# Kernel tuning notes

Measured on AMD Instinct MI355X. Metric: run time of the kernel, lower is better.

Reference implementation:

```python
import jax, jax.numpy as jnp
import numpy as np

N, E, F, H, EA = 50000, 640000, 128, 128, 8


def setup_inputs() -> dict:
    key = jax.random.key(0)
    ks = jax.random.split(key, 16)
    s = 0.05
    return {
        "h": jax.random.normal(ks[0], (N, F), jnp.float32),
        "pos": jax.random.normal(ks[1], (N, 3), jnp.float32),
        "edge_index": jax.random.randint(ks[2], (2, E), 0, N, jnp.int32),
        "edge_attr": jax.random.normal(ks[3], (E, EA), jnp.float32),
        # edge_mlp_1: in = 2F + 1 + EA
        "eW1": jax.random.normal(ks[4], (2 * F + 1 + EA, H), jnp.float32) * s,
        "eb1": jnp.zeros((H,), jnp.float32),
        "eW2": jax.random.normal(ks[5], (H, H), jnp.float32) * s,
        "eb2": jnp.zeros((H,), jnp.float32),
        "aW": jax.random.normal(ks[6], (H, 1), jnp.float32) * s,
        "ab": jnp.zeros((1,), jnp.float32),
        "nW1": jax.random.normal(ks[7], (H + F, H), jnp.float32) * s,
        "nb1": jnp.zeros((H,), jnp.float32),
        "nW2": jax.random.normal(ks[8], (H, F), jnp.float32) * s,
        "nb2": jnp.zeros((F,), jnp.float32),
        # pos_mlp_2: xavier with gain 0.001 -> tiny init, no bias
        "pW2": jax.random.normal(ks[9], (H, 1), jnp.float32) * 0.001,
    }


def reference(h, pos, edge_index, edge_attr,
              eW1, eb1, eW2, eb2, aW, ab,
              nW1, nb1, nW2, nb2, pW2):
    n = h.shape[0]
    row, col = edge_index[0], edge_index[1]
    # radial info
    pos_diff = pos[row] - pos[col]                      # [E,3]
    dist_sq = jnp.sum(pos_diff * pos_diff, axis=-1, keepdims=True)  # [E,1]
    # edge model (Eq.3): gather -> MLP -> sigmoid attention gate
    e_in = jnp.concatenate([h[row], h[col], dist_sq, edge_attr], axis=-1)
    m = jax.nn.silu(e_in @ eW1 + eb1)
    m = jax.nn.silu(m @ eW2 + eb2)
    m = m * jax.nn.sigmoid(m @ aW + ab)                 # [E,H]
    # pos model (note: original overwrites pos_mlp_1 output; faithful to that)
    trans = pos_diff * (m @ pW2)                        # [E,3]
    agg_t = jax.ops.segment_sum(trans, row, num_segments=n)
    cnt = jax.ops.segment_sum(jnp.ones((trans.shape[0], 1), trans.dtype), row,
                              num_segments=n)
    pos_new = pos + agg_t / jnp.maximum(cnt, 1.0)       # unsorted_segment_mean
    # node model: scatter-sum aggregate -> MLP -> residual
    agg = jax.ops.segment_sum(m, row, num_segments=n)   # [N,H]
    o = jax.nn.silu(jnp.concatenate([h, agg], axis=1) @ nW1 + nb1)
    h_new = o @ nW2 + nb2 + h
    return h_new, pos_new, m
```

## Files before the change

### kernel.cpp

```cpp
#include <hip/hip_runtime.h>
#include <hip/hip_bf16.h>

#define NN 50000
#define EE 640000
#define FF 128
#define HH 128

typedef unsigned short ushort_t;
typedef unsigned int   uint_t;
using f32x4  = __attribute__((ext_vector_type(4))) float;
using bf16x8 = __attribute__((ext_vector_type(8))) __bf16;
using u16x8  = __attribute__((ext_vector_type(8))) unsigned short;

__device__ __forceinline__ ushort_t f2bf(float f) {
    union { float f; unsigned int i; } v; v.f = f;
    unsigned int r = v.i + 0x7fffu + ((v.i >> 16) & 1u);
    return (ushort_t)(r >> 16);
}
__device__ __forceinline__ float bf2f(uint_t u) {
    union { uint_t i; float f; } v; v.i = u << 16; return v.f;
}
__device__ __forceinline__ float fsilu(float x) { return x / (1.f + __expf(-x)); }
__device__ __forceinline__ float fsig(float x)  { return 1.f / (1.f + __expf(-x)); }

__device__ __forceinline__ u16x8 cvt8(const float* p) {
    float4 a0 = *reinterpret_cast<const float4*>(p);
    float4 a1 = *reinterpret_cast<const float4*>(p + 4);
    u16x8 v;
    v[0] = f2bf(a0.x); v[1] = f2bf(a0.y); v[2] = f2bf(a0.z); v[3] = f2bf(a0.w);
    v[4] = f2bf(a1.x); v[5] = f2bf(a1.y); v[6] = f2bf(a1.z); v[7] = f2bf(a1.w);
    return v;
}

__device__ __forceinline__ void gld_lds16(const void* g, void* l) {
    typedef const __attribute__((address_space(1))) unsigned int glb_u32;
    typedef __attribute__((address_space(3))) unsigned int lds_u32;
    __builtin_amdgcn_global_load_lds((glb_u32*)g, (lds_u32*)l, 16, 0, 0);
}

__global__ void prep_kernel(const float* __restrict__ h, ushort_t* __restrict__ hbf,
                            const int* __restrict__ eidx, int* __restrict__ deg)
{
    const int t = blockIdx.x * 256 + threadIdx.x;
    if (t * 8 < NN * 128) {
        u16x8 v = cvt8(h + (size_t)t * 8);
        *reinterpret_cast<u16x8*>(hbf + (size_t)t * 8) = v;
    }
    if (t < EE) atomicAdd(&deg[eidx[t]], 1);
}

__global__ void scan_kernel(const int* __restrict__ deg, int* __restrict__ row_ptr,
                            int* __restrict__ cursor)
{
    __shared__ int sdata[1024];
    const int t = threadIdx.x;
    const int chunk = (NN + 1023) / 1024;
    const int start = t * chunk;
    const int end   = min(start + chunk, NN);
    int s = 0;
    for (int i = start; i < end; ++i) s += deg[i];
    sdata[t] = s;
    __syncthreads();
    for (int off = 1; off < 1024; off <<= 1) {
        int v = (t >= off) ? sdata[t - off] : 0;
        __syncthreads();
        sdata[t] += v;
        __syncthreads();
    }
    int ox = sdata[t] - s;
    for (int i = start; i < end; ++i) {
        row_ptr[i] = ox; cursor[i] = ox; ox += deg[i];
    }
    if (t == 1023) row_ptr[NN] = sdata[1023];
}

__global__ void scatter_kernel(const int* __restrict__ eidx, int* __restrict__ cursor,
                               int* __restrict__ edge_list, int* __restrict__ row_sorted)
{
    const int e = blockIdx.x * 256 + threadIdx.x;
    if (e < EE) {
        const int r = eidx[e];
        const int p = atomicAdd(&cursor[r], 1);
        edge_list[p] = e;
        row_sorted[p] = r;
    }
}

#define M_STR 136

__device__ __forceinline__ ushort_t* ah_ptr(ushort_t* base, int row, int b) {
    return base + row * 256 + ((b ^ ((row & 7) << 4)) >> 1);
}

__global__ __launch_bounds__(256, 2) void egcl_edge_kernel(
    const ushort_t* __restrict__ hbf, const float* __restrict__ pos,
    const int* __restrict__ eidx, const float* __restrict__ eattr,
    const int* __restrict__ edge_list, const int* __restrict__ row_sorted,
    const float* __restrict__ w1, const float* __restrict__ b1,
    const float* __restrict__ w2, const float* __restrict__ b2,
    const float* __restrict__ aW, const float* __restrict__ ab,
    const float* __restrict__ pW2,
    float* __restrict__ m_out, float* __restrict__ agg, float* __restrict__ agg_t)
{
    __shared__ __align__(16) ushort_t A_h[64 * 256];
    __shared__ __align__(16) ushort_t A_misc[64 * 16];
    __shared__ __align__(16) ushort_t M1_sh[64 * M_STR];
    __shared__ int   ROW_sh[64];
    __shared__ float GATE_sh[64];

    ushort_t* M2_sh = A_h;

    const int tid  = threadIdx.x;
    const int lane = tid & 63;
    const int w    = tid >> 6;
    const int l15  = lane & 15;
    const int lg   = lane >> 4;

    bf16x8 B1[9][2];
    bf16x8 B2[4][2];
    bf16x8 Bg[4];
    float b1c[2], b2c[2];
    const float abv = ab[0];
#pragma unroll
    for (int nt = 0; nt < 2; ++nt) {
        const int colg = 32 * w + 16 * nt + l15;
        b1c[nt] = b1[colg];
        b2c[nt] = b2[colg];
#pragma unroll
        for (int ks = 0; ks < 9; ++ks) {
            u16x8 v;
#pragma unroll
            for (int j = 0; j < 8; ++j) {
                const int k = 32 * ks + 8 * lg + j;
                v[j] = (k < 265) ? f2bf(w1[k * 128 + colg]) : (ushort_t)0;
            }
            B1[ks][nt] = __builtin_bit_cast(bf16x8, v);
        }
#pragma unroll
        for (int ks = 0; ks < 4; ++ks) {
            u16x8 v;
#pragma unroll
            for (int j = 0; j < 8; ++j) {
                const int k = 32 * ks + 8 * lg + j;
                v[j] = f2bf(w2[k * 128 + colg]);
            }
            B2[ks][nt] = __builtin_bit_cast(bf16x8, v);
        }
    }
#pragma unroll
    for (int ks = 0; ks < 4; ++ks) {
        u16x8 v;
#pragma unroll
        for (int j = 0; j < 8; ++j) {
            const int k = 32 * ks + 8 * lg + j;
            v[j] = (l15 == 0) ? f2bf(aW[k]) : (l15 == 1 ? f2bf(pW2[k]) : (ushort_t)0);
        }
        Bg[ks] = __builtin_bit_cast(bf16x8, v);
    }

    const int ei = tid >> 2;
    const int et = tid & 3;

    for (int tile = blockIdx.x; tile < EE / 64; tile += gridDim.x) {
        const int p  = tile * 64 + ei;
        const int eo = edge_list[p];
        const int r  = row_sorted[p];
        const int c  = eidx[EE + eo];

#pragma unroll
        for (int i = 0; i < 8; ++i) {
            const int rl = 2 * i + (lane >> 5);
            const int bs = (lane & 31) << 4;
            const int b  = bs ^ ((rl & 7) << 4);
            const int rr = __shfl(r, 4 * rl);
            const int cc = __shfl(c, 4 * rl);
            const int node = (b < 256) ? rr : cc;
            const char* src = (const char*)hbf + (size_t)node * 256 + (b & 255);
            gld_lds16(src, (char*)A_h + (w * 8192 + i * 1024));
        }

        float pdx = 0.f, pdy = 0.f, pdz = 0.f;
        if (et == 0) {
            ROW_sh[ei] = r;
            pdx = pos[r * 3 + 0] - pos[c * 3 + 0];
            pdy = pos[r * 3 + 1] - pos[c * 3 + 1];
            pdz = pos[r * 3 + 2] - pos[c * 3 + 2];
            const float ds = pdx * pdx + pdy * pdy + pdz * pdz;
            const float4 ea0 = *reinterpret_cast<const float4*>(eattr + (size_t)eo * 8);
            const float4 ea1 = *reinterpret_cast<const float4*>(eattr + (size_t)eo * 8 + 4);
            u16x8 v0;
            v0[0] = f2bf(ds);
            v0[1] = f2bf(ea0.x); v0[2] = f2bf(ea0.y); v0[3] = f2bf(ea0.z);
            v0[4] = f2bf(ea0.w); v0[5] = f2bf(ea1.x); v0[6] = f2bf(ea1.y);
            v0[7] = f2bf(ea1.z);
            *reinterpret_cast<u16x8*>(&A_misc[ei * 16]) = v0;
            u16x8 v1 = {0, 0, 0, 0, 0, 0, 0, 0};
            v1[0] = f2bf(ea1.w);
            *reinterpret_cast<u16x8*>(&A_misc[ei * 16 + 8]) = v1;
        }
        __syncthreads();

#pragma unroll
        for (int s = 0; s < 4; ++s) {
            f32x4 a0 = {0.f, 0.f, 0.f, 0.f};
            f32x4 a1 = {0.f, 0.f, 0.f, 0.f};
#pragma unroll
            for (int ks = 0; ks < 9; ++ks) {
                bf16x8 a;
                if (ks < 8) {
                    a = *reinterpret_cast<const bf16x8*>(
                        ah_ptr(A_h, 16 * s + l15, 64 * ks + 16 * lg));
                } else if (lg < 2) {
                    a = *reinterpret_cast<const bf16x8*>(
                        &A_misc[(16 * s + l15) * 16 + 8 * lg]);
                } else {
                    u16x8 z = {0, 0, 0, 0, 0, 0, 0, 0};
                    a = __builtin_bit_cast(bf16x8, z);
                }
                a0 = __builtin_amdgcn_mfma_f32_16x16x32_bf16(a, B1[ks][0], a0, 0, 0, 0);
                a1 = __builtin_amdgcn_mfma_f32_16x16x32_bf16(a, B1[ks][1], a1, 0, 0, 0);
            }
#pragma unroll
            for (int nt = 0; nt < 2; ++nt) {
#pragma unroll
                for (int rr2 = 0; rr2 < 4; ++rr2) {
                    const float x = (nt == 0 ? a0[rr2] : a1[rr2]) + b1c[nt];
                    const int edge = 16 * s + 4 * lg + rr2;
                    const int colg = 32 * w + 16 * nt + l15;
                    M1_sh[edge * M_STR + colg] = f2bf(fsilu(x));
                }
            }
        }
        __syncthreads();

#pragma unroll
        for (int s = 0; s < 4; ++s) {
            f32x4 a0 = {0.f, 0.f, 0.f, 0.f};
            f32x4 a1 = {0.f, 0.f, 0.f, 0.f};
#pragma unroll
            for (int ks = 0; ks < 4; ++ks) {
                bf16x8 a = *reinterpret_cast<const bf16x8*>(
                    &M1_sh[(16 * s + l15) * M_STR + ks * 32 + lg * 8]);
                a0 = __builtin_amdgcn_mfma_f32_16x16x32_bf16(a, B2[ks][0], a0, 0, 0, 0);
                a1 = __builtin_amdgcn_mfma_f32_16x16x32_bf16(a, B2[ks][1], a1, 0, 0, 0);
            }
#pragma unroll
            for (int nt = 0; nt < 2; ++nt) {
#pragma unroll
                for (int rr2 = 0; rr2 < 4; ++rr2) {
                    const float x = (nt == 0 ? a0[rr2] : a1[rr2]) + b2c[nt];
                    const int edge = 16 * s + 4 * lg + rr2;
                    const int colg = 32 * w + 16 * nt + l15;
                    M2_sh[edge * M_STR + colg] = f2bf(fsilu(x));
                }
            }
        }
        __syncthreads();

        {
            f32x4 ga = {0.f, 0.f, 0.f, 0.f};
#pragma unroll
            for (int ks = 0; ks < 4; ++ks) {
                bf16x8 a = *reinterpret_cast<const bf16x8*>(
                    &M2_sh[(16 * w + l15) * M_STR + ks * 32 + lg * 8]);
                ga = __builtin_amdgcn_mfma_f32_16x16x32_bf16(a, Bg[ks], ga, 0, 0, 0);
            }
            float gqw[4], txw[4], tyw[4], tzw[4];
#pragma unroll
            for (int rr2 = 0; rr2 < 4; ++rr2) {
                const float sa = __shfl(ga[rr2], lane & 48);
                const float sp = __shfl(ga[rr2], (lane & 48) + 1);
                gqw[rr2] = fsig(sa + abv);
                const float t = gqw[rr2] * sp;
                const float px = __shfl(pdx, 16 * lg + 4 * rr2);
                const float py = __shfl(pdy, 16 * lg + 4 * rr2);
                const float pz = __shfl(pdz, 16 * lg + 4 * rr2);
                txw[rr2] = px * t; tyw[rr2] = py * t; tzw[rr2] = pz * t;
                if (l15 == 0) GATE_sh[16 * w + 4 * lg + rr2] = gqw[rr2];
            }
            if (l15 == 0) {
                int cur = -1; float t0 = 0.f, t1 = 0.f, t2 = 0.f;
#pragma unroll
                for (int rr2 = 0; rr2 < 4; ++rr2) {
                    const int rid = ROW_sh[16 * w + 4 * lg + rr2];
                    if (rid != cur) {
                        if (cur >= 0) {
                            atomicAdd(&agg_t[cur * 3 + 0], t0);
                            atomicAdd(&agg_t[cur * 3 + 1], t1);
                            atomicAdd(&agg_t[cur * 3 + 2], t2);
                        }
                        cur = rid; t0 = t1 = t2 = 0.f;
                    }
                    t0 += txw[rr2]; t1 += tyw[rr2]; t2 += tzw[rr2];
                }
                atomicAdd(&agg_t[cur * 3 + 0], t0);
                atomicAdd(&agg_t[cur * 3 + 1], t1);
                atomicAdd(&agg_t[cur * 3 + 2], t2);
            }
        }
        __syncthreads();

#pragma unroll
        for (int j = 0; j < 16; ++j) {
            const int row = 16 * w + j;
            const int eo2 = edge_list[tile * 64 + row];
            const uint_t pv = *reinterpret_cast<const uint_t*>(&M2_sh[row * M_STR + 2 * lane]);
            const float g = GATE_sh[row];
            float2 st;
            st.x = bf2f(pv & 0xffffu) * g;
            st.y = bf2f(pv >> 16) * g;
            *reinterpret_cast<float2*>(&m_out[(size_t)eo2 * 128 + 2 * lane]) = st;
        }

        {
            const int col = tid & 127;
            const int j0  = (tid >> 7) * 32;
            int cur = ROW_sh[j0];
            float acc = 0.f;
#pragma unroll 4
            for (int j = j0; j < j0 + 32; ++j) {
                const int rid = ROW_sh[j];
                const float v = bf2f((uint_t)M2_sh[j * M_STR + col]) * GATE_sh[j];
                if (rid != cur) {
                    atomicAdd(&agg[(size_t)cur * 128 + col], acc);
                    acc = 0.f; cur = rid;
                }
                acc += v;
            }
            atomicAdd(&agg[(size_t)cur * 128 + col], acc);
        }
        __syncthreads();
    }
}

__global__ __launch_bounds__(256, 4) void egcl_node_kernel(
    const ushort_t* __restrict__ hbf,
    const float* __restrict__ agg, const float* __restrict__ agg_t,
    const int* __restrict__ row_ptr, const float* __restrict__ pos,
    const float* __restrict__ w1, const float* __restrict__ b1,
    const float* __restrict__ w2, const float* __restrict__ b2,
    float* __restrict__ hn_out, float* __restrict__ pos_out)
{
    __shared__ __align__(16) ushort_t A_sh[16 * 264];
    __shared__ __align__(16) ushort_t M1_sh[16 * 136];

    const int tid  = threadIdx.x;
    const int lane = tid & 63;
    const int w    = tid >> 6;
    const int l15  = lane & 15;
    const int lg   = lane >> 4;

    bf16x8 B1[8][2];
    bf16x8 B2[4][2];
    float b1c[2], b2c[2];
#pragma unroll
    for (int nt = 0; nt < 2; ++nt) {
        const int colg = 32 * w + 16 * nt + l15;
        b1c[nt] = b1[colg];
        b2c[nt] = b2[colg];
#pragma unroll
        for (int ks = 0; ks < 8; ++ks) {
            u16x8 v;
#pragma unroll
            for (int j = 0; j < 8; ++j) {
                const int k = 32 * ks + 8 * lg + j;
                v[j] = f2bf(w1[k * 128 + colg]);
            }
            B1[ks][nt] = __builtin_bit_cast(bf16x8, v);
        }
#pragma unroll
        for (int ks = 0; ks < 4; ++ks) {
            u16x8 v;
#pragma unroll
            for (int j = 0; j < 8; ++j) {
                const int k = 32 * ks + 8 * lg + j;
                v[j] = f2bf(w2[k * 128 + colg]);
            }
            B2[ks][nt] = __builtin_bit_cast(bf16x8, v);
        }
    }

    const int ni = tid >> 4;
    const int nt16 = tid & 15;

    for (int tile = blockIdx.x; tile < NN / 16; tile += gridDim.x) {
        __syncthreads();
        const int base = tile * 16;
        {
            const size_t n = (size_t)base + ni;
            *reinterpret_cast<u16x8*>(&A_sh[ni * 264 + nt16 * 8]) =
                *reinterpret_cast<const u16x8*>(hbf + n * 128 + nt16 * 8);
            u16x8 av = cvt8(agg + n * 128 + nt16 * 8);
            *reinterpret_cast<u16x8*>(&A_sh[ni * 264 + 128 + nt16 * 8]) = av;
        }
        if (tid < 48) {
            const int nl = tid / 3, d = tid % 3;
            const size_t n = (size_t)base + nl;
            const float c = (float)(row_ptr[n + 1] - row_ptr[n]);
            pos_out[n * 3 + d] = pos[n * 3 + d] + agg_t[n * 3 + d] / fmaxf(c, 1.f);
        }
        __syncthreads();

        f32x4 acc10 = {0.f, 0.f, 0.f, 0.f};
        f32x4 acc11 = {0.f, 0.f, 0.f, 0.f};
#pragma unroll
        for (int ks = 0; ks < 8; ++ks) {
            bf16x8 a = *reinterpret_cast<const bf16x8*>(&A_sh[l15 * 264 + ks * 32 + lg * 8]);
            acc10 = __builtin_amdgcn_mfma_f32_16x16x32_bf16(a, B1[ks][0], acc10, 0, 0, 0);
            acc11 = __builtin_amdgcn_mfma_f32_16x16x32_bf16(a, B1[ks][1], acc11, 0, 0, 0);
        }
#pragma unroll
        for (int nt = 0; nt < 2; ++nt) {
#pragma unroll
            for (int r = 0; r < 4; ++r) {
                const float x = (nt == 0 ? acc10[r] : acc11[r]) + b1c[nt];
                const int nl = 4 * lg + r;
                const int colg = 32 * w + 16 * nt + l15;
                M1_sh[nl * 136 + colg] = f2bf(fsilu(x));
            }
        }
        __syncthreads();

        f32x4 acc20 = {0.f, 0.f, 0.f, 0.f};
        f32x4 acc21 = {0.f, 0.f, 0.f, 0.f};
#pragma unroll
        for (int ks = 0; ks < 4; ++ks) {
            bf16x8 a = *reinterpret_cast<const bf16x8*>(&M1_sh[l15 * 136 + ks * 32 + lg * 8]);
            acc20 = __builtin_amdgcn_mfma_f32_16x16x32_bf16(a, B2[ks][0], acc20, 0, 0, 0);
            acc21 = __builtin_amdgcn_mfma_f32_16x16x32_bf16(a, B2[ks][1], acc21, 0, 0, 0);
        }
#pragma unroll
        for (int nt = 0; nt < 2; ++nt) {
#pragma unroll
            for (int r = 0; r < 4; ++r) {
                const int nl = 4 * lg + r;
                const int colg = 32 * w + 16 * nt + l15;
                const size_t n = (size_t)base + nl;
                const float hres = bf2f((uint_t)A_sh[nl * 264 + colg]);
                const float y = (nt == 0 ? acc20[r] : acc21[r]) + b2c[nt] + hres;
                hn_out[n * 128 + colg] = y;
            }
        }
    }
}

extern "C" void kernel_launch(void* const* d_in, const int* in_sizes, int n_in,
                              void* d_out, int out_size, void* d_ws, size_t ws_size,
                              hipStream_t stream)
{
    const float* h     = (const float*)d_in[0];
    const float* pos   = (const float*)d_in[1];
    const int*   eidx  = (const int*)d_in[2];
    const float* eattr = (const float*)d_in[3];
    const float* eW1   = (const float*)d_in[4];
    const float* eb1   = (const float*)d_in[5];
    const float* eW2   = (const float*)d_in[6];
    const float* eb2   = (const float*)d_in[7];
    const float* aW    = (const float*)d_in[8];
    const float* ab    = (const float*)d_in[9];
    const float* nW1   = (const float*)d_in[10];
    const float* nb1   = (const float*)d_in[11];
    const float* nW2   = (const float*)d_in[12];
    const float* nb2   = (const float*)d_in[13];
    const float* pW2   = (const float*)d_in[14];

    float* out    = (float*)d_out;
    float* hn_out = out;
    float* po_out = out + (size_t)NN * 128;
    float* m_out  = po_out + (size_t)NN * 3;

    char* wsb = (char*)d_ws;
    float* agg        = (float*)(wsb + 0);
    float* agg_t      = (float*)(wsb + 25600000);
    int*   deg        = (int*)  (wsb + 26200000);
    int*   row_ptr    = (int*)  (wsb + 26400000);
    int*   cursor     = (int*)  (wsb + 26600256);
    int*   edge_list  = (int*)  (wsb + 26800256);
    int*   row_sorted = (int*)  (wsb + 29360256);
    ushort_t* hbf     = (ushort_t*)(wsb + 31920256);

    hipMemsetAsync(wsb, 0, 26400000, stream);

    prep_kernel<<<3200, 256, 0, stream>>>(h, hbf, eidx, deg);
    scan_kernel<<<1, 1024, 0, stream>>>(deg, row_ptr, cursor);
    scatter_kernel<<<(EE + 255) / 256, 256, 0, stream>>>(eidx, cursor, edge_list, row_sorted);

    egcl_edge_kernel<<<512, 256, 0, stream>>>(hbf, pos, eidx, eattr,
                                              edge_list, row_sorted,
                                              eW1, eb1, eW2, eb2, aW, ab, pW2,
                                              m_out, agg, agg_t);
    egcl_node_kernel<<<512, 256, 0, stream>>>(hbf, agg, agg_t, row_ptr, pos,
                                              nW1, nb1, nW2, nb2,
                                              hn_out, po_out);
}
```

Baseline: 519.0 us.

## Prefetch next edge tile, parallelize scan, fold agg zeroing into prep

The single-block serial prefix scan becomes a three-kernel parallel scan. Zeroing agg moves from a large memset into prep_kernel, so the memset only clears agg_t and deg. The edge kernel now issues the next tile's gather loads (do_stage) at the end of each iteration, overlapping them with compute. It also drops a barrier by fusing the m_out store with per-wave segmented atomic aggregation, and lays out M2_sh in per-wave blocks. The changes remove serial scan latency and memset traffic and hide gather latency. The cost is more launches and extra live registers for the prefetched pos_diff values.

```diff
diff --git a/kernel.cpp b/kernel.cpp
--- a/kernel.cpp
+++ b/kernel.cpp
@@ -39,39 +39,65 @@
 }
 
 __global__ void prep_kernel(const float* __restrict__ h, ushort_t* __restrict__ hbf,
-                            const int* __restrict__ eidx, int* __restrict__ deg)
+                            const int* __restrict__ eidx, int* __restrict__ deg,
+                            float* __restrict__ agg)
 {
     const int t = blockIdx.x * 256 + threadIdx.x;
-    if (t * 8 < NN * 128) {
+    if (t < 800000) {
         u16x8 v = cvt8(h + (size_t)t * 8);
         *reinterpret_cast<u16x8*>(hbf + (size_t)t * 8) = v;
+        const float4 z4 = {0.f, 0.f, 0.f, 0.f};
+        *reinterpret_cast<float4*>(agg + (size_t)t * 8)     = z4;
+        *reinterpret_cast<float4*>(agg + (size_t)t * 8 + 4) = z4;
     }
     if (t < EE) atomicAdd(&deg[eidx[t]], 1);
 }
 
-__global__ void scan_kernel(const int* __restrict__ deg, int* __restrict__ row_ptr,
-                            int* __restrict__ cursor)
-{
-    __shared__ int sdata[1024];
+__global__ void scan_local_kernel(const int* __restrict__ deg,
+                                  int* __restrict__ row_ptr, int* __restrict__ bsum)
+{
+    __shared__ int sd[256];
     const int t = threadIdx.x;
-    const int chunk = (NN + 1023) / 1024;
-    const int start = t * chunk;
-    const int end   = min(start + chunk, NN);
-    int s = 0;
-    for (int i = start; i < end; ++i) s += deg[i];
-    sdata[t] = s;
+    const int i = blockIdx.x * 256 + t;
+    const int v = (i < NN) ? deg[i] : 0;
+    sd[t] = v;
     __syncthreads();
-    for (int off = 1; off < 1024; off <<= 1) {
-        int v = (t >= off) ? sdata[t - off] : 0;
-        __syncthreads();
-        sdata[t] += v;
-        __syncthreads();
-    }
-    int ox = sdata[t] - s;
-    for (int i = start; i < end; ++i) {
-        row_ptr[i] = ox; cursor[i] = ox; ox += deg[i];
-    }
-    if (t == 1023) row_ptr[NN] = sdata[1023];
+    for (int off = 1; off < 256; off <<= 1) {
+        const int u = (t >= off) ? sd[t - off] : 0;
+        __syncthreads();
+        sd[t] += u;
+        __syncthreads();
+    }
+    if (i < NN) row_ptr[i] = sd[t] - v;
+    if (t == 255) bsum[blockIdx.x] = sd[255];
+}
+
+__global__ void scan_bsum_kernel(int* __restrict__ bsum)
+{
+    __shared__ int sd[256];
+    const int t = threadIdx.x;
+    const int v = (t < 196) ? bsum[t] : 0;
+    sd[t] = v;
+    __syncthreads();
+    for (int off = 1; off < 256; off <<= 1) {
+        const int u = (t >= off) ? sd[t - off] : 0;
+        __syncthreads();
+        sd[t] += u;
+        __syncthreads();
+    }
+    if (t < 196) bsum[t] = sd[t] - v;
+}
+
+__global__ void scan_fix_kernel(int* __restrict__ row_ptr, const int* __restrict__ bsum,
+                                int* __restrict__ cursor)
+{
+    const int i = blockIdx.x * 256 + threadIdx.x;
+    if (i < NN) {
+        const int p = row_ptr[i] + bsum[blockIdx.x];
+        row_ptr[i] = p;
+        cursor[i]  = p;
+    }
+    if (i == 0) row_ptr[NN] = EE;
 }
 
 __global__ void scatter_kernel(const int* __restrict__ eidx, int* __restrict__ cursor,
@@ -90,6 +116,9 @@
 
 __device__ __forceinline__ ushort_t* ah_ptr(ushort_t* base, int row, int b) {
     return base + row * 256 + ((b ^ ((row & 7) << 4)) >> 1);
+}
+__device__ __forceinline__ int m2_off(int row) {
+    return (row >> 4) * 4096 + (row & 15) * M_STR;
 }
 
 __global__ __launch_bounds__(256, 2) void egcl_edge_kernel(
@@ -160,13 +189,15 @@
 
     const int ei = tid >> 2;
     const int et = tid & 3;
-
-    for (int tile = blockIdx.x; tile < EE / 64; tile += gridDim.x) {
-        const int p  = tile * 64 + ei;
+    const int NT = EE / 64;
+
+    float pdx = 0.f, pdy = 0.f, pdz = 0.f;
+
+    auto do_stage = [&](int t) {
+        const int p  = t * 64 + ei;
         const int eo = edge_list[p];
         const int r  = row_sorted[p];
         const int c  = eidx[EE + eo];
-
 #pragma unroll
         for (int i = 0; i < 8; ++i) {
             const int rl = 2 * i + (lane >> 5);
@@ -178,8 +209,6 @@
             const char* src = (const char*)hbf + (size_t)node * 256 + (b & 255);
             gld_lds16(src, (char*)A_h + (w * 8192 + i * 1024));
         }
-
-        float pdx = 0.f, pdy = 0.f, pdz = 0.f;
         if (et == 0) {
             ROW_sh[ei] = r;
             pdx = pos[r * 3 + 0] - pos[c * 3 + 0];
@@ -198,6 +227,11 @@
             v1[0] = f2bf(ea1.w);
             *reinterpret_cast<u16x8*>(&A_misc[ei * 16 + 8]) = v1;
         }
+    };
+
+    do_stage(blockIdx.x);
+
+    for (int tile = blockIdx.x; tile < NT; tile += gridDim.x) {
         __syncthreads();
 
 #pragma unroll
@@ -251,7 +285,7 @@
                     const float x = (nt == 0 ? a0[rr2] : a1[rr2]) + b2c[nt];
                     const int edge = 16 * s + 4 * lg + rr2;
                     const int colg = 32 * w + 16 * nt + l15;
-                    M2_sh[edge * M_STR + colg] = f2bf(fsilu(x));
+                    M2_sh[m2_off(edge) + colg] = f2bf(fsilu(x));
                 }
             }
         }
@@ -262,7 +296,7 @@
 #pragma unroll
             for (int ks = 0; ks < 4; ++ks) {
                 bf16x8 a = *reinterpret_cast<const bf16x8*>(
-                    &M2_sh[(16 * w + l15) * M_STR + ks * 32 + lg * 8]);
+                    &M2_sh[m2_off(16 * w + l15) + ks * 32 + lg * 8]);
                 ga = __builtin_amdgcn_mfma_f32_16x16x32_bf16(a, Bg[ks], ga, 0, 0, 0);
             }
             float gqw[4], txw[4], tyw[4], tzw[4];
@@ -298,38 +332,37 @@
                 atomicAdd(&agg_t[cur * 3 + 2], t2);
             }
         }
-        __syncthreads();
-
-#pragma unroll
-        for (int j = 0; j < 16; ++j) {
-            const int row = 16 * w + j;
-            const int eo2 = edge_list[tile * 64 + row];
-            const uint_t pv = *reinterpret_cast<const uint_t*>(&M2_sh[row * M_STR + 2 * lane]);
-            const float g = GATE_sh[row];
-            float2 st;
-            st.x = bf2f(pv & 0xffffu) * g;
-            st.y = bf2f(pv >> 16) * g;
-            *reinterpret_cast<float2*>(&m_out[(size_t)eo2 * 128 + 2 * lane]) = st;
-        }
 
         {
-            const int col = tid & 127;
-            const int j0  = (tid >> 7) * 32;
-            int cur = ROW_sh[j0];
-            float acc = 0.f;
-#pragma unroll 4
-            for (int j = j0; j < j0 + 32; ++j) {
-                const int rid = ROW_sh[j];
-                const float v = bf2f((uint_t)M2_sh[j * M_STR + col]) * GATE_sh[j];
+            float ax = 0.f, ay = 0.f;
+            int cur = ROW_sh[16 * w];
+#pragma unroll
+            for (int j = 0; j < 16; ++j) {
+                const int row = 16 * w + j;
+                const int rid = ROW_sh[row];
+                const int eo2 = edge_list[tile * 64 + row];
+                const uint_t pv = *reinterpret_cast<const uint_t*>(
+                    &M2_sh[m2_off(row) + 2 * lane]);
+                const float g = GATE_sh[row];
+                float2 st;
+                st.x = bf2f(pv & 0xffffu) * g;
+                st.y = bf2f(pv >> 16) * g;
+                *reinterpret_cast<float2*>(&m_out[(size_t)eo2 * 128 + 2 * lane]) = st;
                 if (rid != cur) {
-                    atomicAdd(&agg[(size_t)cur * 128 + col], acc);
-                    acc = 0.f; cur = rid;
+                    atomicAdd(&agg[(size_t)cur * 128 + 2 * lane],     ax);
+                    atomicAdd(&agg[(size_t)cur * 128 + 2 * lane + 1], ay);
+                    cur = rid; ax = 0.f; ay = 0.f;
                 }
-                acc += v;
-            }
-            atomicAdd(&agg[(size_t)cur * 128 + col], acc);
-        }
-        __syncthreads();
+                ax += st.x; ay += st.y;
+            }
+            atomicAdd(&agg[(size_t)cur * 128 + 2 * lane],     ax);
+            atomicAdd(&agg[(size_t)cur * 128 + 2 * lane + 1], ay);
+        }
+
+        asm volatile("s_waitcnt lgkmcnt(0)" ::: "memory");
+        __builtin_amdgcn_sched_barrier(0);
+        const int nxt = tile + gridDim.x;
+        if (nxt < NT) do_stage(nxt);
     }
 }
 
@@ -470,19 +503,22 @@
     float* m_out  = po_out + (size_t)NN * 3;
 
     char* wsb = (char*)d_ws;
-    float* agg        = (float*)(wsb + 0);
-    float* agg_t      = (float*)(wsb + 25600000);
-    int*   deg        = (int*)  (wsb + 26200000);
-    int*   row_ptr    = (int*)  (wsb + 26400000);
-    int*   cursor     = (int*)  (wsb + 26600256);
-    int*   edge_list  = (int*)  (wsb + 26800256);
-    int*   row_sorted = (int*)  (wsb + 29360256);
-    ushort_t* hbf     = (ushort_t*)(wsb + 31920256);
-
-    hipMemsetAsync(wsb, 0, 26400000, stream);
-
-    prep_kernel<<<3200, 256, 0, stream>>>(h, hbf, eidx, deg);
-    scan_kernel<<<1, 1024, 0, stream>>>(deg, row_ptr, cursor);
+    float* agg_t      = (float*)(wsb + 0);
+    int*   deg        = (int*)  (wsb + 600064);
+    int*   row_ptr    = (int*)  (wsb + 800064);
+    int*   cursor     = (int*)  (wsb + 1000320);
+    int*   bsum       = (int*)  (wsb + 1200320);
+    int*   edge_list  = (int*)  (wsb + 1201152);
+    int*   row_sorted = (int*)  (wsb + 3761152);
+    ushort_t* hbf     = (ushort_t*)(wsb + 6321152);
+    float* agg        = (float*)(wsb + 19121408);
+
+    hipMemsetAsync(wsb, 0, 800064, stream);
+
+    prep_kernel<<<3200, 256, 0, stream>>>(h, hbf, eidx, deg, agg);
+    scan_local_kernel<<<196, 256, 0, stream>>>(deg, row_ptr, bsum);
+    scan_bsum_kernel<<<1, 256, 0, stream>>>(bsum);
+    scan_fix_kernel<<<196, 256, 0, stream>>>(row_ptr, bsum, cursor);
     scatter_kernel<<<(EE + 255) / 256, 256, 0, stream>>>(eidx, cursor, edge_list, row_sorted);
 
     egcl_edge_kernel<<<512, 256, 0, stream>>>(hbf, pos, eidx, eattr,
```

Result: faster. 432.1 us (median of 2 runs) (-16.7%).
